# Kernel optimization log

Measured on AMD Instinct MI355X. Metric: run time of the kernel, lower is better.

The kernel has to match this reference:

```python
import jax, jax.numpy as jnp
import numpy as np

FEATURE_DIM = 512
PREDICATE_DIM = 2000
OBJECT_DIM = 100000
BATCH = 131072
EPS = 1e-5


def setup_inputs() -> dict:
    key = jax.random.key(0)
    ks = jax.random.split(key, 20)
    f, f2 = FEATURE_DIM, FEATURE_DIM // 2

    def w(k, shape, fan_in):
        bound = 1.0 / np.sqrt(fan_in)
        return jax.random.uniform(k, shape, jnp.float32, -bound, bound)

    inp = {
        "subj": jax.random.randint(ks[0], (BATCH,), 0, OBJECT_DIM),
        "obj": jax.random.randint(ks[1], (BATCH,), 0, OBJECT_DIM),
        "predi": jax.random.randint(ks[2], (BATCH,), 0, PREDICATE_DIM),
        # Linear weights stored as (in, out) so one_hot @ W.T == W_io[idx]
        "W1": w(ks[3], (OBJECT_DIM, f), OBJECT_DIM), "b1": w(ks[4], (f,), OBJECT_DIM),
        "g1": jnp.ones((f,), jnp.float32), "be1": jnp.zeros((f,), jnp.float32),
        "W2": w(ks[5], (OBJECT_DIM, f), OBJECT_DIM), "b2": w(ks[6], (f,), OBJECT_DIM),
        "g2": jnp.ones((f,), jnp.float32), "be2": jnp.zeros((f,), jnp.float32),
        "W3": w(ks[7], (PREDICATE_DIM, f), PREDICATE_DIM), "b3": w(ks[8], (f,), PREDICATE_DIM),
        "g3": jnp.ones((f,), jnp.float32), "be3": jnp.zeros((f,), jnp.float32),
        "W4": w(ks[9], (f2, f), f), "b4": w(ks[10], (f2,), f),
        "g4": jnp.ones((f2,), jnp.float32), "be4": jnp.zeros((f2,), jnp.float32),
        "W5": w(ks[11], (1, f2), f2), "b5": w(ks[12], (1,), f2),
    }
    return inp


def _bn(x, g, b):
    # BatchNorm1d training mode: biased variance over batch
    m = jnp.mean(x, axis=0)
    v = jnp.var(x, axis=0)
    return g * (x - m) * jax.lax.rsqrt(v + EPS) + b


def reference(subj, obj, predi,
              W1, b1, g1, be1,
              W2, b2, g2, be2,
              W3, b3, g3, be3,
              W4, b4, g4, be4,
              W5, b5):
    # one_hot(idx) @ W.T + b  ==  row gather of (in,out) weight
    s = jax.nn.relu(_bn(W1[subj] + b1, g1, be1))
    o = jax.nn.relu(_bn(W2[obj] + b2, g2, be2))
    p = jax.nn.relu(_bn(W3[predi] + b3, g3, be3))
    fused = s + p + o                                  # [B, F]
    h = jax.nn.relu(_bn(fused @ W4.T + b4, g4, be4))   # [B, F//2]
    logit = (h @ W5.T + b5).squeeze()                  # [B]
    return logit
```

## Files before the change

kernel.cpp:

```cpp
#include <hip/hip_runtime.h>

#define BATCHN 131072
#define FD 512
#define F2 256
#define NOBJ 100000
#define NPRED 2000
#define LDSTR 520
#define RPB 128

typedef __bf16 bf16x8 __attribute__((ext_vector_type(8)));
typedef float f32x4 __attribute__((ext_vector_type(4)));

__device__ __forceinline__ ushort f2bf(float f) {
  union { float f; uint u; } c; c.f = f;
  uint u = c.u;
  u += 0x7FFFu + ((u >> 16) & 1u);
  return (ushort)(u >> 16);
}

#define WS_STATS123 202752
#define WS_S4       205824
#define WS_SCSH123  238592
#define WS_SCSH4    241664
#define WS_W4BF     242176
#define WS_WBF1     307712
#define WS_WBF2     25907712
#define WS_WBF3     51507712
#define WS_A1       52019712
#define WS_A2       64819712
#define WS_A3       77619712
#define WS_H        WS_WBF1

__global__ __launch_bounds__(256) void k_hist(
    const int* __restrict__ subj, const int* __restrict__ obj,
    const int* __restrict__ predi, int* __restrict__ cnt)
{
  int b = blockIdx.x * 256 + threadIdx.x;
  atomicAdd(&cnt[subj[b]], 1);
  atomicAdd(&cnt[NOBJ + obj[b]], 1);
  atomicAdd(&cnt[2 * NOBJ + predi[b]], 1);
}

__global__ __launch_bounds__(256) void k_scanconv(
    const float* __restrict__ W, const int* __restrict__ cn,
    float* __restrict__ statsE, ushort* __restrict__ wbf, int N)
{
  __shared__ float redS[512], redQ[512];
  int t = threadIdx.x;
  redS[t] = 0.f; redS[t + 256] = 0.f; redQ[t] = 0.f; redQ[t + 256] = 0.f;
  __syncthreads();
  int c = t & 63, rg = t >> 6;
  int base = blockIdx.x * RPB;
  int end = min(N, base + RPB);
  float s[8], q[8];
  #pragma unroll
  for (int j = 0; j < 8; ++j) { s[j] = 0.f; q[j] = 0.f; }

  #pragma unroll 4
  for (int r = base + rg; r < end; r += 4) {
    const float* row = W + (size_t)r * FD + c * 8;
    float4 va = *(const float4*)(row);
    float4 vb = *(const float4*)(row + 4);
    float wv = (float)cn[r];
    float x[8] = {va.x, va.y, va.z, va.w, vb.x, vb.y, vb.z, vb.w};
    union { ushort o[8]; uint4 v; } u;
    #pragma unroll
    for (int j = 0; j < 8; ++j) {
      float wx = wv * x[j];
      s[j] += wx; q[j] = fmaf(wx, x[j], q[j]);
      u.o[j] = f2bf(x[j]);
    }
    if (wv > 0.f) *(uint4*)&wbf[(size_t)r * FD + c * 8] = u.v;
  }

  #pragma unroll
  for (int j = 0; j < 8; ++j) {
    atomicAdd(&redS[c * 8 + j], s[j]);
    atomicAdd(&redQ[c * 8 + j], q[j]);
  }
  __syncthreads();
  atomicAdd(&statsE[t],        redS[t]);
  atomicAdd(&statsE[t + 256],  redS[t + 256]);
  atomicAdd(&statsE[512 + t],  redQ[t]);
  atomicAdd(&statsE[768 + t],  redQ[t + 256]);
}

__global__ void k_fin123(const float* __restrict__ stats,
                         const float* __restrict__ g1, const float* __restrict__ be1,
                         const float* __restrict__ g2, const float* __restrict__ be2,
                         const float* __restrict__ g3, const float* __restrict__ be3,
                         float* __restrict__ scsh)
{
  int e = blockIdx.x, f = threadIdx.x;
  const float* g  = (e == 0) ? g1  : (e == 1 ? g2  : g3);
  const float* be = (e == 0) ? be1 : (e == 1 ? be2 : be3);
  float S = stats[e * 1024 + f], SS = stats[e * 1024 + 512 + f];
  const float invB = 1.f / (float)BATCHN;
  float mean = S * invB;
  float var  = SS * invB - mean * mean;
  if (!(var >= 0.f && var < 1e30f)) var = 1.f;
  if (!(mean > -1e30f && mean < 1e30f)) mean = 0.f;
  float r = rsqrtf(var + 1e-5f);
  float sc = g[f] * r;
  scsh[e * 1024 + f]       = sc;
  scsh[e * 1024 + 512 + f] = be[f] - mean * sc;
}

__global__ __launch_bounds__(256) void k_convW4(const float* __restrict__ W4,
                                                ushort* __restrict__ w4bf)
{
  int i = (blockIdx.x * 256 + threadIdx.x) * 4;
  float4 v = *(const float4*)(W4 + i);
  ushort4 o = {f2bf(v.x), f2bf(v.y), f2bf(v.z), f2bf(v.w)};
  *(ushort4*)(w4bf + i) = o;
}

__global__ __launch_bounds__(256, 4) void k_gemmA(
    const ushort* __restrict__ wbf, const ushort* __restrict__ w4bf,
    const int* __restrict__ cn, const float* __restrict__ scshE,
    ushort* __restrict__ A, int N)
{
  alignas(16) __shared__ ushort tileL[32 * LDSTR];
  __shared__ int cnOk[32];
  int t = threadIdx.x;
  int rowBase = blockIdx.x * 32;
  int c = t & 63, rg = t >> 6;
  int w = t >> 6, lane = t & 63, m = lane & 15, q = lane >> 4;

  if (t < 32) { int gr = rowBase + t; cnOk[t] = (gr < N) && (cn[gr] != 0); }

  uint4 st[8];
  #pragma unroll
  for (int u = 0; u < 8; ++u) {
    int gr = rowBase + rg + 4 * u; if (gr >= N) gr = N - 1;
    st[u] = *(const uint4*)&wbf[(size_t)gr * FD + c * 8];
  }
  const ushort* w4p = w4bf + ((size_t)(64 * w + m)) * FD + q * 8;
  bf16x8 bc0 = *(const bf16x8*)(w4p + 0 * 16 * FD);
  bf16x8 bc1 = *(const bf16x8*)(w4p + 1 * 16 * FD);
  bf16x8 bc2 = *(const bf16x8*)(w4p + 2 * 16 * FD);
  bf16x8 bc3 = *(const bf16x8*)(w4p + 3 * 16 * FD);

  float sc[8], sh[8];
  #pragma unroll
  for (int j = 0; j < 8; ++j) {
    sc[j] = scshE[c * 8 + j];
    sh[j] = scshE[512 + c * 8 + j];
  }

  #pragma unroll
  for (int u = 0; u < 8; ++u) {
    int r = rg + 4 * u;
    union { uint4 v; ushort o[8]; } in; in.v = st[u];
    union { ushort o[8]; uint4 v; } out;
    #pragma unroll
    for (int j = 0; j < 8; ++j) {
      union { uint uu; float f; } cv; cv.uu = (uint)in.o[j] << 16;
      float v = fmaxf(fmaf(sc[j], cv.f, sh[j]), 0.f);
      v = fminf(v, 60000.f);
      out.o[j] = f2bf(v);
    }
    *(uint4*)&tileL[r * LDSTR + c * 8] = out.v;
  }
  __syncthreads();

  f32x4 acc[2][4];
  #pragma unroll
  for (int mi = 0; mi < 2; ++mi)
    #pragma unroll
    for (int ni = 0; ni < 4; ++ni)
      acc[mi][ni] = (f32x4){0.f, 0.f, 0.f, 0.f};
  const ushort* fpL = tileL + m * LDSTR + q * 8;

  for (int kk = 0; kk < 16; ++kk) {
    int kc = kk * 32;
    bf16x8 af0 = *(const bf16x8*)(fpL + kc);
    bf16x8 af1 = *(const bf16x8*)(fpL + 16 * LDSTR + kc);
    bf16x8 bn0, bn1, bn2, bn3;
    if (kk < 15) {
      int kn = kc + 32;
      bn0 = *(const bf16x8*)(w4p + 0 * 16 * FD + kn);
      bn1 = *(const bf16x8*)(w4p + 1 * 16 * FD + kn);
      bn2 = *(const bf16x8*)(w4p + 2 * 16 * FD + kn);
      bn3 = *(const bf16x8*)(w4p + 3 * 16 * FD + kn);
    }
    acc[0][0] = __builtin_amdgcn_mfma_f32_16x16x32_bf16(af0, bc0, acc[0][0], 0, 0, 0);
    acc[1][0] = __builtin_amdgcn_mfma_f32_16x16x32_bf16(af1, bc0, acc[1][0], 0, 0, 0);
    acc[0][1] = __builtin_amdgcn_mfma_f32_16x16x32_bf16(af0, bc1, acc[0][1], 0, 0, 0);
    acc[1][1] = __builtin_amdgcn_mfma_f32_16x16x32_bf16(af1, bc1, acc[1][1], 0, 0, 0);
    acc[0][2] = __builtin_amdgcn_mfma_f32_16x16x32_bf16(af0, bc2, acc[0][2], 0, 0, 0);
    acc[1][2] = __builtin_amdgcn_mfma_f32_16x16x32_bf16(af1, bc2, acc[1][2], 0, 0, 0);
    acc[0][3] = __builtin_amdgcn_mfma_f32_16x16x32_bf16(af0, bc3, acc[0][3], 0, 0, 0);
    acc[1][3] = __builtin_amdgcn_mfma_f32_16x16x32_bf16(af1, bc3, acc[1][3], 0, 0, 0);
    bc0 = bn0; bc1 = bn1; bc2 = bn2; bc3 = bn3;
  }
  __syncthreads();

  ushort* ldsB = (ushort*)tileL;
  #pragma unroll
  for (int mi = 0; mi < 2; ++mi)
    #pragma unroll
    for (int ni = 0; ni < 4; ++ni)
      #pragma unroll
      for (int rr = 0; rr < 4; ++rr)
        ldsB[(16 * mi + 4 * q + rr) * 268 + 64 * w + 16 * ni + m] = f2bf(acc[mi][ni][rr]);
  __syncthreads();
  int hr = t >> 7, p = (t & 127) * 2;
  #pragma unroll
  for (int r = 0; r < 32; r += 2) {
    int rr = r + hr;
    if (cnOk[rr])
      *(uint*)&A[(size_t)(rowBase + rr) * F2 + p] = *(const uint*)&ldsB[rr * 268 + p];
  }
}

__global__ __launch_bounds__(256) void k_hstats(
    const int* __restrict__ subj, const int* __restrict__ obj,
    const int* __restrict__ predi,
    const ushort* __restrict__ A1, const ushort* __restrict__ A2,
    const ushort* __restrict__ A3, ushort* __restrict__ h,
    float* __restrict__ s4)
{
  __shared__ float colS[256], colQ[256];
  int t = threadIdx.x;
  colS[t] = 0.f; colQ[t] = 0.f;
  __syncthreads();
  int c = t & 31;
  int pair = t >> 5;
  float ls[8], lq[8];
  #pragma unroll
  for (int j = 0; j < 8; ++j) { ls[j] = 0.f; lq[j] = 0.f; }
  int base = blockIdx.x * 64;
  #pragma unroll 4
  for (int i = 0; i < 8; ++i) {
    int b = base + i * 8 + pair;
    bf16x8 v1 = *(const bf16x8*)(A1 + (size_t)subj[b]  * F2 + c * 8);
    bf16x8 v2 = *(const bf16x8*)(A2 + (size_t)obj[b]   * F2 + c * 8);
    bf16x8 v3 = *(const bf16x8*)(A3 + (size_t)predi[b] * F2 + c * 8);
    union { ushort o[8]; uint4 v; } u;
    #pragma unroll
    for (int j = 0; j < 8; ++j) {
      float hv = (float)v1[j] + (float)v2[j] + (float)v3[j];
      ls[j] += hv; lq[j] = fmaf(hv, hv, lq[j]);
      u.o[j] = f2bf(hv);
    }
    *(uint4*)&h[(size_t)b * F2 + c * 8] = u.v;
  }
  #pragma unroll
  for (int j = 0; j < 8; ++j) {
    atomicAdd(&colS[c * 8 + j], ls[j]);
    atomicAdd(&colQ[c * 8 + j], lq[j]);
  }
  __syncthreads();
  int slot = blockIdx.x & 63;
  atomicAdd(&s4[slot * 512 + t],       colS[t]);
  atomicAdd(&s4[slot * 512 + 256 + t], colQ[t]);
}

__global__ void k_fin4(const float* __restrict__ s4, const float* __restrict__ g4,
                       const float* __restrict__ be4, float* __restrict__ scsh4)
{
  int j = threadIdx.x;
  float S = 0.f, SS = 0.f;
  for (int sl = 0; sl < 64; ++sl) { S += s4[sl * 512 + j]; SS += s4[sl * 512 + 256 + j]; }
  const float invB = 1.f / (float)BATCHN;
  float mean = S * invB;
  float var  = SS * invB - mean * mean;
  if (!(var >= 0.f && var < 1e30f)) var = 1.f;
  if (!(mean > -1e30f && mean < 1e30f)) mean = 0.f;
  float r = rsqrtf(var + 1e-5f);
  float sc = g4[j] * r;
  scsh4[j]       = sc;
  scsh4[256 + j] = be4[j] - mean * sc;
}

__global__ __launch_bounds__(256) void k_final(
    const ushort* __restrict__ h, const float* __restrict__ scsh4,
    const float* __restrict__ W5, const float* __restrict__ b5,
    float* __restrict__ out)
{
  int t = threadIdx.x;
  int c = t & 31, pair = t >> 5;
  float sc4v[8], sh4v[8], w5v[8];
  #pragma unroll
  for (int j = 0; j < 8; ++j) {
    int col = c * 8 + j;
    sc4v[j] = scsh4[col];
    sh4v[j] = scsh4[256 + col];
    w5v[j]  = W5[col];
  }
  float bb = b5[0];
  int base = blockIdx.x * 64;
  #pragma unroll 4
  for (int i = 0; i < 8; ++i) {
    int b = base + i * 8 + pair;
    bf16x8 hv = *(const bf16x8*)(h + (size_t)b * F2 + c * 8);
    float acc = 0.f;
    #pragma unroll
    for (int j = 0; j < 8; ++j)
      acc += fmaxf(fmaf(sc4v[j], (float)hv[j], sh4v[j]), 0.f) * w5v[j];
    #pragma unroll
    for (int off = 1; off < 32; off <<= 1)
      acc += __shfl_xor(acc, off, 64);
    if (c == 0) out[b] = acc + bb;
  }
}

extern "C" void kernel_launch(void* const* d_in, const int* in_sizes, int n_in,
                              void* d_out, int out_size, void* d_ws, size_t ws_size,
                              hipStream_t stream)
{
  const int* subj  = (const int*)d_in[0];
  const int* obj   = (const int*)d_in[1];
  const int* predi = (const int*)d_in[2];
  const float* W1  = (const float*)d_in[3];
  const float* g1  = (const float*)d_in[5];
  const float* be1 = (const float*)d_in[6];
  const float* W2  = (const float*)d_in[7];
  const float* g2  = (const float*)d_in[9];
  const float* be2 = (const float*)d_in[10];
  const float* W3  = (const float*)d_in[11];
  const float* g3  = (const float*)d_in[13];
  const float* be3 = (const float*)d_in[14];
  const float* W4  = (const float*)d_in[15];
  const float* g4  = (const float*)d_in[17];
  const float* be4 = (const float*)d_in[18];
  const float* W5  = (const float*)d_in[19];
  const float* b5  = (const float*)d_in[20];

  float* wsf   = (float*)d_ws;
  int*   cnt   = (int*)d_ws;
  ushort* w4bf = (ushort*)(wsf + WS_W4BF);
  ushort* wbf1 = (ushort*)(wsf + WS_WBF1);
  ushort* wbf2 = (ushort*)(wsf + WS_WBF2);
  ushort* wbf3 = (ushort*)(wsf + WS_WBF3);
  ushort* A1   = (ushort*)(wsf + WS_A1);
  ushort* A2   = (ushort*)(wsf + WS_A2);
  ushort* A3   = (ushort*)(wsf + WS_A3);
  ushort* hbuf = (ushort*)(wsf + WS_H);
  float* out   = (float*)d_out;

  hipMemsetAsync(d_ws, 0, WS_SCSH123 * 4, stream);
  k_hist<<<BATCHN / 256, 256, 0, stream>>>(subj, obj, predi, cnt);
  k_convW4<<<128, 256, 0, stream>>>(W4, w4bf);

  k_scanconv<<<(NOBJ + RPB - 1) / RPB, 256, 0, stream>>>(W1, cnt, wsf + WS_STATS123, wbf1, NOBJ);
  k_scanconv<<<(NOBJ + RPB - 1) / RPB, 256, 0, stream>>>(W2, cnt + NOBJ, wsf + WS_STATS123 + 1024, wbf2, NOBJ);
  k_scanconv<<<(NPRED + RPB - 1) / RPB, 256, 0, stream>>>(W3, cnt + 2 * NOBJ, wsf + WS_STATS123 + 2048, wbf3, NPRED);
  k_fin123<<<3, 512, 0, stream>>>(wsf + WS_STATS123, g1, be1, g2, be2, g3, be3, wsf + WS_SCSH123);

  k_gemmA<<<NOBJ / 32, 256, 0, stream>>>(wbf1, w4bf, cnt, wsf + WS_SCSH123, A1, NOBJ);
  k_gemmA<<<NOBJ / 32, 256, 0, stream>>>(wbf2, w4bf, cnt + NOBJ, wsf + WS_SCSH123 + 1024, A2, NOBJ);
  k_gemmA<<<(NPRED + 31) / 32, 256, 0, stream>>>(wbf3, w4bf, cnt + 2 * NOBJ, wsf + WS_SCSH123 + 2048, A3, NPRED);

  k_hstats<<<BATCHN / 64, 256, 0, stream>>>(subj, obj, predi, A1, A2, A3, hbuf, wsf + WS_S4);
  k_fin4<<<1, 256, 0, stream>>>(wsf + WS_S4, g4, be4, wsf + WS_SCSH4);
  k_final<<<BATCHN / 64, 256, 0, stream>>>(hbuf, wsf + WS_SCSH4, W5, b5, out);
}
```

Baseline: 894.5 us.

## Split BN-ReLU into separate pass and load GEMM tiles directly into LDS

```diff
diff --git a/kernel.cpp b/kernel.cpp
--- a/kernel.cpp
+++ b/kernel.cpp
@@ -16,6 +16,12 @@
   uint u = c.u;
   u += 0x7FFFu + ((u >> 16) & 1u);
   return (ushort)(u >> 16);
+}
+
+__device__ __forceinline__ void gload16(const void* g, void* l) {
+  __builtin_amdgcn_global_load_lds(
+      (const __attribute__((address_space(1))) void*)g,
+      (__attribute__((address_space(3))) void*)l, 16, 0, 0);
 }
 
 #define WS_STATS123 202752
@@ -41,9 +47,9 @@
   atomicAdd(&cnt[2 * NOBJ + predi[b]], 1);
 }
 
-__global__ __launch_bounds__(256) void k_scanconv(
+__global__ __launch_bounds__(256) void k_scan(
     const float* __restrict__ W, const int* __restrict__ cn,
-    float* __restrict__ statsE, ushort* __restrict__ wbf, int N)
+    float* __restrict__ statsE, int N)
 {
   __shared__ float redS[512], redQ[512];
   int t = threadIdx.x;
@@ -63,14 +69,11 @@
     float4 vb = *(const float4*)(row + 4);
     float wv = (float)cn[r];
     float x[8] = {va.x, va.y, va.z, va.w, vb.x, vb.y, vb.z, vb.w};
-    union { ushort o[8]; uint4 v; } u;
     #pragma unroll
     for (int j = 0; j < 8; ++j) {
       float wx = wv * x[j];
       s[j] += wx; q[j] = fmaf(wx, x[j], q[j]);
-      u.o[j] = f2bf(x[j]);
     }
-    if (wv > 0.f) *(uint4*)&wbf[(size_t)r * FD + c * 8] = u.v;
   }
 
   #pragma unroll
@@ -106,6 +109,38 @@
   scsh[e * 1024 + 512 + f] = be[f] - mean * sc;
 }
 
+__global__ __launch_bounds__(256) void k_bnrelu(
+    const float* __restrict__ W, const int* __restrict__ cn,
+    const float* __restrict__ scshE, ushort* __restrict__ wbf, int N)
+{
+  int t = threadIdx.x;
+  int c = t & 63, rg = t >> 6;
+  float sc[8], sh[8];
+  #pragma unroll
+  for (int j = 0; j < 8; ++j) {
+    sc[j] = scshE[c * 8 + j];
+    sh[j] = scshE[512 + c * 8 + j];
+  }
+  int base = blockIdx.x * RPB;
+  int end = min(N, base + RPB);
+  #pragma unroll 4
+  for (int r = base + rg; r < end; r += 4) {
+    if (cn[r] == 0) continue;
+    const float* row = W + (size_t)r * FD + c * 8;
+    float4 va = *(const float4*)(row);
+    float4 vb = *(const float4*)(row + 4);
+    float x[8] = {va.x, va.y, va.z, va.w, vb.x, vb.y, vb.z, vb.w};
+    union { ushort o[8]; uint4 v; } u;
+    #pragma unroll
+    for (int j = 0; j < 8; ++j) {
+      float v = fmaxf(fmaf(sc[j], x[j], sh[j]), 0.f);
+      v = fminf(v, 60000.f);
+      u.o[j] = f2bf(v);
+    }
+    *(uint4*)&wbf[(size_t)r * FD + c * 8] = u.v;
+  }
+}
+
 __global__ __launch_bounds__(256) void k_convW4(const float* __restrict__ W4,
                                                 ushort* __restrict__ w4bf)
 {
@@ -115,53 +150,30 @@
   *(ushort4*)(w4bf + i) = o;
 }
 
-__global__ __launch_bounds__(256, 4) void k_gemmA(
+__global__ __launch_bounds__(256) void k_gemmA(
     const ushort* __restrict__ wbf, const ushort* __restrict__ w4bf,
-    const int* __restrict__ cn, const float* __restrict__ scshE,
-    ushort* __restrict__ A, int N)
+    const int* __restrict__ cn, ushort* __restrict__ A, int N)
 {
   alignas(16) __shared__ ushort tileL[32 * LDSTR];
   __shared__ int cnOk[32];
   int t = threadIdx.x;
   int rowBase = blockIdx.x * 32;
-  int c = t & 63, rg = t >> 6;
   int w = t >> 6, lane = t & 63, m = lane & 15, q = lane >> 4;
 
   if (t < 32) { int gr = rowBase + t; cnOk[t] = (gr < N) && (cn[gr] != 0); }
 
-  uint4 st[8];
   #pragma unroll
   for (int u = 0; u < 8; ++u) {
-    int gr = rowBase + rg + 4 * u; if (gr >= N) gr = N - 1;
-    st[u] = *(const uint4*)&wbf[(size_t)gr * FD + c * 8];
-  }
+    int r = w + 4 * u;
+    int gr = rowBase + r; if (gr >= N) gr = N - 1;
+    gload16(wbf + (size_t)gr * FD + lane * 8, &tileL[r * LDSTR]);
+  }
+
   const ushort* w4p = w4bf + ((size_t)(64 * w + m)) * FD + q * 8;
   bf16x8 bc0 = *(const bf16x8*)(w4p + 0 * 16 * FD);
   bf16x8 bc1 = *(const bf16x8*)(w4p + 1 * 16 * FD);
   bf16x8 bc2 = *(const bf16x8*)(w4p + 2 * 16 * FD);
   bf16x8 bc3 = *(const bf16x8*)(w4p + 3 * 16 * FD);
-
-  float sc[8], sh[8];
-  #pragma unroll
-  for (int j = 0; j < 8; ++j) {
-    sc[j] = scshE[c * 8 + j];
-    sh[j] = scshE[512 + c * 8 + j];
-  }
-
-  #pragma unroll
-  for (int u = 0; u < 8; ++u) {
-    int r = rg + 4 * u;
-    union { uint4 v; ushort o[8]; } in; in.v = st[u];
-    union { ushort o[8]; uint4 v; } out;
-    #pragma unroll
-    for (int j = 0; j < 8; ++j) {
-      union { uint uu; float f; } cv; cv.uu = (uint)in.o[j] << 16;
-      float v = fmaxf(fmaf(sc[j], cv.f, sh[j]), 0.f);
-      v = fminf(v, 60000.f);
-      out.o[j] = f2bf(v);
-    }
-    *(uint4*)&tileL[r * LDSTR + c * 8] = out.v;
-  }
   __syncthreads();
 
   f32x4 acc[2][4];
@@ -344,14 +356,18 @@
   k_hist<<<BATCHN / 256, 256, 0, stream>>>(subj, obj, predi, cnt);
   k_convW4<<<128, 256, 0, stream>>>(W4, w4bf);
 
-  k_scanconv<<<(NOBJ + RPB - 1) / RPB, 256, 0, stream>>>(W1, cnt, wsf + WS_STATS123, wbf1, NOBJ);
-  k_scanconv<<<(NOBJ + RPB - 1) / RPB, 256, 0, stream>>>(W2, cnt + NOBJ, wsf + WS_STATS123 + 1024, wbf2, NOBJ);
-  k_scanconv<<<(NPRED + RPB - 1) / RPB, 256, 0, stream>>>(W3, cnt + 2 * NOBJ, wsf + WS_STATS123 + 2048, wbf3, NPRED);
+  k_scan<<<(NOBJ + RPB - 1) / RPB, 256, 0, stream>>>(W1, cnt, wsf + WS_STATS123, NOBJ);
+  k_scan<<<(NOBJ + RPB - 1) / RPB, 256, 0, stream>>>(W2, cnt + NOBJ, wsf + WS_STATS123 + 1024, NOBJ);
+  k_scan<<<(NPRED + RPB - 1) / RPB, 256, 0, stream>>>(W3, cnt + 2 * NOBJ, wsf + WS_STATS123 + 2048, NPRED);
   k_fin123<<<3, 512, 0, stream>>>(wsf + WS_STATS123, g1, be1, g2, be2, g3, be3, wsf + WS_SCSH123);
 
-  k_gemmA<<<NOBJ / 32, 256, 0, stream>>>(wbf1, w4bf, cnt, wsf + WS_SCSH123, A1, NOBJ);
-  k_gemmA<<<NOBJ / 32, 256, 0, stream>>>(wbf2, w4bf, cnt + NOBJ, wsf + WS_SCSH123 + 1024, A2, NOBJ);
-  k_gemmA<<<(NPRED + 31) / 32, 256, 0, stream>>>(wbf3, w4bf, cnt + 2 * NOBJ, wsf + WS_SCSH123 + 2048, A3, NPRED);
+  k_bnrelu<<<(NOBJ + RPB - 1) / RPB, 256, 0, stream>>>(W1, cnt, wsf + WS_SCSH123, wbf1, NOBJ);
+  k_bnrelu<<<(NOBJ + RPB - 1) / RPB, 256, 0, stream>>>(W2, cnt + NOBJ, wsf + WS_SCSH123 + 1024, wbf2, NOBJ);
+  k_bnrelu<<<(NPRED + RPB - 1) / RPB, 256, 0, stream>>>(W3, cnt + 2 * NOBJ, wsf + WS_SCSH123 + 2048, wbf3, NPRED);
+
+  k_gemmA<<<NOBJ / 32, 256, 0, stream>>>(wbf1, w4bf, cnt, A1, NOBJ);
+  k_gemmA<<<NOBJ / 32, 256, 0, stream>>>(wbf2, w4bf, cnt + NOBJ, A2, NOBJ);
+  k_gemmA<<<(NPRED + 31) / 32, 256, 0, stream>>>(wbf3, w4bf, cnt + 2 * NOBJ, A3, NPRED);
 
   k_hstats<<<BATCHN / 64, 256, 0, stream>>>(subj, obj, predi, A1, A2, A3, hbuf, wsf + WS_S4);
   k_fin4<<<1, 256, 0, stream>>>(wsf + WS_S4, g4, be4, wsf + WS_SCSH4);
```

Measured after the change: 979.7 us. 1.1x slower.

## Split BN+ReLU into in-place pass and retile W4 GEMM with LDS double-buffering

Applied to the files above, without the earlier changes.

```diff
diff --git a/kernel.cpp b/kernel.cpp
--- a/kernel.cpp
+++ b/kernel.cpp
@@ -5,8 +5,9 @@
 #define F2 256
 #define NOBJ 100000
 #define NPRED 2000
-#define LDSTR 520
 #define RPB 128
+#define GR 128
+#define GK 32
 
 typedef __bf16 bf16x8 __attribute__((ext_vector_type(8)));
 typedef float f32x4 __attribute__((ext_vector_type(4)));
@@ -16,6 +17,12 @@
   uint u = c.u;
   u += 0x7FFFu + ((u >> 16) & 1u);
   return (ushort)(u >> 16);
+}
+
+__device__ __forceinline__ void gload16(const void* g, void* l) {
+  __builtin_amdgcn_global_load_lds(
+      (const __attribute__((address_space(1))) void*)g,
+      (__attribute__((address_space(3))) void*)l, 16, 0, 0);
 }
 
 #define WS_STATS123 202752
@@ -106,52 +113,25 @@
   scsh[e * 1024 + 512 + f] = be[f] - mean * sc;
 }
 
-__global__ __launch_bounds__(256) void k_convW4(const float* __restrict__ W4,
-                                                ushort* __restrict__ w4bf)
-{
-  int i = (blockIdx.x * 256 + threadIdx.x) * 4;
-  float4 v = *(const float4*)(W4 + i);
-  ushort4 o = {f2bf(v.x), f2bf(v.y), f2bf(v.z), f2bf(v.w)};
-  *(ushort4*)(w4bf + i) = o;
-}
-
-__global__ __launch_bounds__(256, 4) void k_gemmA(
-    const ushort* __restrict__ wbf, const ushort* __restrict__ w4bf,
+__global__ __launch_bounds__(256) void k_bnrelu2(
     const int* __restrict__ cn, const float* __restrict__ scshE,
-    ushort* __restrict__ A, int N)
-{
-  alignas(16) __shared__ ushort tileL[32 * LDSTR];
-  __shared__ int cnOk[32];
-  int t = threadIdx.x;
-  int rowBase = blockIdx.x * 32;
+    ushort* __restrict__ wbf, int N)
+{
+  int t = threadIdx.x;
   int c = t & 63, rg = t >> 6;
-  int w = t >> 6, lane = t & 63, m = lane & 15, q = lane >> 4;
-
-  if (t < 32) { int gr = rowBase + t; cnOk[t] = (gr < N) && (cn[gr] != 0); }
-
-  uint4 st[8];
-  #pragma unroll
-  for (int u = 0; u < 8; ++u) {
-    int gr = rowBase + rg + 4 * u; if (gr >= N) gr = N - 1;
-    st[u] = *(const uint4*)&wbf[(size_t)gr * FD + c * 8];
-  }
-  const ushort* w4p = w4bf + ((size_t)(64 * w + m)) * FD + q * 8;
-  bf16x8 bc0 = *(const bf16x8*)(w4p + 0 * 16 * FD);
-  bf16x8 bc1 = *(const bf16x8*)(w4p + 1 * 16 * FD);
-  bf16x8 bc2 = *(const bf16x8*)(w4p + 2 * 16 * FD);
-  bf16x8 bc3 = *(const bf16x8*)(w4p + 3 * 16 * FD);
-
   float sc[8], sh[8];
   #pragma unroll
   for (int j = 0; j < 8; ++j) {
     sc[j] = scshE[c * 8 + j];
     sh[j] = scshE[512 + c * 8 + j];
   }
-
-  #pragma unroll
-  for (int u = 0; u < 8; ++u) {
-    int r = rg + 4 * u;
-    union { uint4 v; ushort o[8]; } in; in.v = st[u];
+  int base = blockIdx.x * RPB;
+  int end = min(N, base + RPB);
+  #pragma unroll 4
+  for (int r = base + rg; r < end; r += 4) {
+    if (cn[r] == 0) continue;
+    ushort* p = wbf + (size_t)r * FD + c * 8;
+    union { uint4 v; ushort o[8]; } in; in.v = *(const uint4*)p;
     union { ushort o[8]; uint4 v; } out;
     #pragma unroll
     for (int j = 0; j < 8; ++j) {
@@ -160,57 +140,108 @@
       v = fminf(v, 60000.f);
       out.o[j] = f2bf(v);
     }
-    *(uint4*)&tileL[r * LDSTR + c * 8] = out.v;
-  }
-  __syncthreads();
-
-  f32x4 acc[2][4];
-  #pragma unroll
-  for (int mi = 0; mi < 2; ++mi)
+    *(uint4*)p = out.v;
+  }
+}
+
+__global__ __launch_bounds__(256) void k_convW4(const float* __restrict__ W4,
+                                                ushort* __restrict__ w4bf)
+{
+  int i = (blockIdx.x * 256 + threadIdx.x) * 4;
+  float4 v = *(const float4*)(W4 + i);
+  ushort4 o = {f2bf(v.x), f2bf(v.y), f2bf(v.z), f2bf(v.w)};
+  *(ushort4*)(w4bf + i) = o;
+}
+
+__global__ __launch_bounds__(512) void k_gemmA(
+    const ushort* __restrict__ wbf, const ushort* __restrict__ w4bf,
+    const int* __restrict__ cn, ushort* __restrict__ A, int N)
+{
+  __shared__ ushort lds[128 * 268];
+  __shared__ int cnOk[128];
+  int t = threadIdx.x;
+  int lane = t & 63, m = lane & 15, q = lane >> 4;
+  int wv = t >> 6, wr = wv >> 2, wc = wv & 3;
+  int rowBase = blockIdx.x * GR;
+
+  if (t < 128) { int gr = rowBase + t; cnOk[t] = (gr < N) && (cn[gr] != 0); }
+
+  f32x4 acc[4][4];
+  #pragma unroll
+  for (int mi = 0; mi < 4; ++mi)
     #pragma unroll
     for (int ni = 0; ni < 4; ++ni)
       acc[mi][ni] = (f32x4){0.f, 0.f, 0.f, 0.f};
-  const ushort* fpL = tileL + m * LDSTR + q * 8;
-
-  for (int kk = 0; kk < 16; ++kk) {
-    int kc = kk * 32;
-    bf16x8 af0 = *(const bf16x8*)(fpL + kc);
-    bf16x8 af1 = *(const bf16x8*)(fpL + 16 * LDSTR + kc);
-    bf16x8 bn0, bn1, bn2, bn3;
-    if (kk < 15) {
-      int kn = kc + 32;
-      bn0 = *(const bf16x8*)(w4p + 0 * 16 * FD + kn);
-      bn1 = *(const bf16x8*)(w4p + 1 * 16 * FD + kn);
-      bn2 = *(const bf16x8*)(w4p + 2 * 16 * FD + kn);
-      bn3 = *(const bf16x8*)(w4p + 3 * 16 * FD + kn);
-    }
-    acc[0][0] = __builtin_amdgcn_mfma_f32_16x16x32_bf16(af0, bc0, acc[0][0], 0, 0, 0);
-    acc[1][0] = __builtin_amdgcn_mfma_f32_16x16x32_bf16(af1, bc0, acc[1][0], 0, 0, 0);
-    acc[0][1] = __builtin_amdgcn_mfma_f32_16x16x32_bf16(af0, bc1, acc[0][1], 0, 0, 0);
-    acc[1][1] = __builtin_amdgcn_mfma_f32_16x16x32_bf16(af1, bc1, acc[1][1], 0, 0, 0);
-    acc[0][2] = __builtin_amdgcn_mfma_f32_16x16x32_bf16(af0, bc2, acc[0][2], 0, 0, 0);
-    acc[1][2] = __builtin_amdgcn_mfma_f32_16x16x32_bf16(af1, bc2, acc[1][2], 0, 0, 0);
-    acc[0][3] = __builtin_amdgcn_mfma_f32_16x16x32_bf16(af0, bc3, acc[0][3], 0, 0, 0);
-    acc[1][3] = __builtin_amdgcn_mfma_f32_16x16x32_bf16(af1, bc3, acc[1][3], 0, 0, 0);
-    bc0 = bn0; bc1 = bn1; bc2 = bn2; bc3 = bn3;
-  }
-  __syncthreads();
-
-  ushort* ldsB = (ushort*)tileL;
-  #pragma unroll
-  for (int mi = 0; mi < 2; ++mi)
+
+  {
+    int kc = 0;
+    { int s = t, row = s >> 2, cc = s & 3;
+      int gr = rowBase + row; if (gr >= N) gr = N - 1;
+      gload16(wbf + (size_t)gr * FD + kc + ((cc ^ (row & 3)) * 8),
+              lds + (size_t)(s & ~63) * 8); }
+    #pragma unroll
+    for (int gg = 0; gg < 2; ++gg) {
+      int s = gg * 512 + t, n = s >> 2, cc = s & 3;
+      gload16(w4bf + (size_t)n * FD + kc + ((cc ^ (n & 3)) * 8),
+              lds + 4096 + (size_t)(s & ~63) * 8);
+    }
+  }
+  __syncthreads();
+
+  for (int ks = 0; ks < 16; ++ks) {
+    int cur = ks & 1;
+    if (ks < 15) {
+      int kc = (ks + 1) * GK;
+      ushort* base = lds + (cur ^ 1) * 12288;
+      { int s = t, row = s >> 2, cc = s & 3;
+        int gr = rowBase + row; if (gr >= N) gr = N - 1;
+        gload16(wbf + (size_t)gr * FD + kc + ((cc ^ (row & 3)) * 8),
+                base + (size_t)(s & ~63) * 8); }
+      #pragma unroll
+      for (int gg = 0; gg < 2; ++gg) {
+        int s = gg * 512 + t, n = s >> 2, cc = s & 3;
+        gload16(w4bf + (size_t)n * FD + kc + ((cc ^ (n & 3)) * 8),
+                base + 4096 + (size_t)(s & ~63) * 8);
+      }
+    }
+    const ushort* abase = lds + cur * 12288;
+    const ushort* bbase = abase + 4096;
+    bf16x8 af[4], bf[4];
+    #pragma unroll
+    for (int mi = 0; mi < 4; ++mi) {
+      int row = wr * 64 + mi * 16 + m;
+      af[mi] = *(const bf16x8*)(abase + (row * 4 + (q ^ (m & 3))) * 8);
+    }
+    #pragma unroll
+    for (int ni = 0; ni < 4; ++ni) {
+      int n = wc * 64 + ni * 16 + m;
+      bf[ni] = *(const bf16x8*)(bbase + (n * 4 + (q ^ (m & 3))) * 8);
+    }
+    #pragma unroll
+    for (int mi = 0; mi < 4; ++mi)
+      #pragma unroll
+      for (int ni = 0; ni < 4; ++ni)
+        acc[mi][ni] = __builtin_amdgcn_mfma_f32_16x16x32_bf16(af[mi], bf[ni], acc[mi][ni], 0, 0, 0);
+    __syncthreads();
+  }
+
+  #pragma unroll
+  for (int mi = 0; mi < 4; ++mi)
     #pragma unroll
     for (int ni = 0; ni < 4; ++ni)
       #pragma unroll
-      for (int rr = 0; rr < 4; ++rr)
-        ldsB[(16 * mi + 4 * q + rr) * 268 + 64 * w + 16 * ni + m] = f2bf(acc[mi][ni][rr]);
-  __syncthreads();
-  int hr = t >> 7, p = (t & 127) * 2;
-  #pragma unroll
-  for (int r = 0; r < 32; r += 2) {
-    int rr = r + hr;
+      for (int rr = 0; rr < 4; ++rr) {
+        int row = wr * 64 + mi * 16 + q * 4 + rr;
+        int col = wc * 64 + ni * 16 + m;
+        lds[row * 268 + col] = f2bf(acc[mi][ni][rr]);
+      }
+  __syncthreads();
+  int sr = t >> 7, p = (t & 127) * 2;
+  #pragma unroll
+  for (int r0 = 0; r0 < 128; r0 += 4) {
+    int rr = r0 + sr;
     if (cnOk[rr])
-      *(uint*)&A[(size_t)(rowBase + rr) * F2 + p] = *(const uint*)&ldsB[rr * 268 + p];
+      *(uint*)&A[(size_t)(rowBase + rr) * F2 + p] = *(const uint*)&lds[rr * 268 + p];
   }
 }
 
@@ -225,8 +256,7 @@
   int t = threadIdx.x;
   colS[t] = 0.f; colQ[t] = 0.f;
   __syncthreads();
-  int c = t & 31;
-  int pair = t >> 5;
+  int c = t & 31, pair = t >> 5;
   float ls[8], lq[8];
   #pragma unroll
   for (int j = 0; j < 8; ++j) { ls[j] = 0.f; lq[j] = 0.f; }
@@ -349,9 +379,13 @@
   k_scanconv<<<(NPRED + RPB - 1) / RPB, 256, 0, stream>>>(W3, cnt + 2 * NOBJ, wsf + WS_STATS123 + 2048, wbf3, NPRED);
   k_fin123<<<3, 512, 0, stream>>>(wsf + WS_STATS123, g1, be1, g2, be2, g3, be3, wsf + WS_SCSH123);
 
-  k_gemmA<<<NOBJ / 32, 256, 0, stream>>>(wbf1, w4bf, cnt, wsf + WS_SCSH123, A1, NOBJ);
-  k_gemmA<<<NOBJ / 32, 256, 0, stream>>>(wbf2, w4bf, cnt + NOBJ, wsf + WS_SCSH123 + 1024, A2, NOBJ);
-  k_gemmA<<<(NPRED + 31) / 32, 256, 0, stream>>>(wbf3, w4bf, cnt + 2 * NOBJ, wsf + WS_SCSH123 + 2048, A3, NPRED);
+  k_bnrelu2<<<(NOBJ + RPB - 1) / RPB, 256, 0, stream>>>(cnt, wsf + WS_SCSH123, wbf1, NOBJ);
+  k_bnrelu2<<<(NOBJ + RPB - 1) / RPB, 256, 0, stream>>>(cnt + NOBJ, wsf + WS_SCSH123 + 1024, wbf2, NOBJ);
+  k_bnrelu2<<<(NPRED + RPB - 1) / RPB, 256, 0, stream>>>(cnt + 2 * NOBJ, wsf + WS_SCSH123 + 2048, wbf3, NPRED);
+
+  k_gemmA<<<(NOBJ + GR - 1) / GR, 512, 0, stream>>>(wbf1, w4bf, cnt, A1, NOBJ);
+  k_gemmA<<<(NOBJ + GR - 1) / GR, 512, 0, stream>>>(wbf2, w4bf, cnt + NOBJ, A2, NOBJ);
+  k_gemmA<<<(NPRED + GR - 1) / GR, 512, 0, stream>>>(wbf3, w4bf, cnt + 2 * NOBJ, A3, NPRED);
 
   k_hstats<<<BATCHN / 64, 256, 0, stream>>>(subj, obj, predi, A1, A2, A3, hbuf, wsf + WS_S4);
   k_fin4<<<1, 256, 0, stream>>>(wsf + WS_S4, g4, be4, wsf + WS_SCSH4);
```

Result: no change. 881.3 us (-1.5%).
